# Performance work log

Measured on AMD Instinct MI355X. Metric: run time of the kernel, lower is better.

The kernel has to match this reference:

```python
import jax, jax.numpy as jnp
import numpy as np

N_NODES = 10000
N_EDGES = 80000
F_IN = 128
H1 = 2048
H2 = 2048
H3 = 1024


def _sgconv(x, pos, src, dst, W_in, b_in, W_out, b_out):
    # geo-GCN SpatialGraphConv with hidden_size=1:
    # message(j->i) = relu(Linear(pos_j - pos_i)) * x_j ; aggr='add' ; then Linear out
    rel = pos[src] - pos[dst]                      # [E, 2]  (pos_j - pos_i)
    scale = jax.nn.relu(rel @ W_in + b_in)         # [E, C_in]
    msg = scale * x[src]                           # [E, C_in]
    agg = jax.ops.segment_sum(msg, dst, num_segments=x.shape[0])  # [N, C_in]
    return agg @ W_out + b_out                     # [N, C_out]


def setup_inputs() -> dict:
    key = jax.random.key(0)
    ks = jax.random.split(key, 12)
    x = jax.random.normal(ks[0], (N_NODES, F_IN), dtype=jnp.float32)
    pos = jax.random.normal(ks[1], (N_NODES, 2), dtype=jnp.float32)
    edge_index = jax.random.randint(ks[2], (2, N_EDGES), 0, N_NODES, dtype=jnp.int32)

    def lin(k, fan_in, fan_out):
        lim = 1.0 / np.sqrt(fan_in)
        kw, kb = jax.random.split(k)
        W = jax.random.uniform(kw, (fan_in, fan_out), jnp.float32, -lim, lim)
        b = jax.random.uniform(kb, (fan_out,), jnp.float32, -lim, lim)
        return W, b

    W_in1, b_in1 = lin(ks[3], 2, F_IN)
    W_out1, b_out1 = lin(ks[4], F_IN, H1)
    W_in2, b_in2 = lin(ks[5], 2, H1)
    W_out2, b_out2 = lin(ks[6], H1, H2)
    W_in3, b_in3 = lin(ks[7], 2, H2)
    W_out3, b_out3 = lin(ks[8], H2, H3)

    return {
        "x": x, "pos": pos, "edge_index": edge_index,
        "W_in1": W_in1, "b_in1": b_in1, "W_out1": W_out1, "b_out1": b_out1,
        "W_in2": W_in2, "b_in2": b_in2, "W_out2": W_out2, "b_out2": b_out2,
        "W_in3": W_in3, "b_in3": b_in3, "W_out3": W_out3, "b_out3": b_out3,
    }


def reference(x, pos, edge_index,
              W_in1, b_in1, W_out1, b_out1,
              W_in2, b_in2, W_out2, b_out2,
              W_in3, b_in3, W_out3, b_out3):
    src, dst = edge_index[0], edge_index[1]  # flow source_to_target: j=src, i=dst
    h = jax.nn.relu(_sgconv(x, pos, src, dst, W_in1, b_in1, W_out1, b_out1))
    h = jax.nn.relu(_sgconv(h, pos, src, dst, W_in2, b_in2, W_out2, b_out2))
    h = jax.nn.relu(_sgconv(h, pos, src, dst, W_in3, b_in3, W_out3, b_out3))
    # F.normalize(h, dim=1): L2 normalize rows with eps clamp 1e-12
    norm = jnp.linalg.norm(h, axis=1, keepdims=True)
    return h / jnp.maximum(norm, 1e-12)
```

## Files before the change

### kernel.cpp

```cpp
#include <hip/hip_runtime.h>
#include <hip/hip_bf16.h>

#define DEVI __device__ __forceinline__

constexpr int NN = 10000;
constexpr int NE = 80000;
constexpr int AGG_ROWS = 10240;
constexpr int ES_CAP = 110016;

typedef __attribute__((ext_vector_type(8))) short bf16x8;
typedef __attribute__((ext_vector_type(4))) float f32x4;

DEVI float blo(unsigned int u) {
  union { unsigned int i; float f; } c; c.i = u << 16; return c.f;
}
DEVI float bhi(unsigned int u) {
  union { unsigned int i; float f; } c; c.i = u & 0xffff0000u; return c.f;
}
DEVI unsigned short f2b(float f) {
  union { float f; unsigned int i; } c; c.f = f;
  unsigned int i = c.i;
  return (unsigned short)((i + 0x7fffu + ((i >> 16) & 1u)) >> 16);
}
DEVI void st1(float* p, float v) { *p = v; }
DEVI void st1(unsigned short* p, float v) { *p = f2b(v); }
DEVI void store8b(unsigned short* p, const float v[8]) {
  int4 pk;
  pk.x = (int)((unsigned)f2b(v[0]) | ((unsigned)f2b(v[1]) << 16));
  pk.y = (int)((unsigned)f2b(v[2]) | ((unsigned)f2b(v[3]) << 16));
  pk.z = (int)((unsigned)f2b(v[4]) | ((unsigned)f2b(v[5]) << 16));
  pk.w = (int)((unsigned)f2b(v[6]) | ((unsigned)f2b(v[7]) << 16));
  *reinterpret_cast<int4*>(p) = pk;
}

DEVI void gload16(const void* g, void* l) {
  __builtin_amdgcn_global_load_lds(
      (const __attribute__((address_space(1))) void*)g,
      (__attribute__((address_space(3))) void*)l, 16, 0, 0);
}

__global__ __launch_bounds__(256)
void hist_kernel(const int* __restrict__ dst, int* __restrict__ cnt) {
  int e = blockIdx.x * 256 + threadIdx.x;
  if (e < NE) atomicAdd(&cnt[dst[e]], 1);
}

__global__ __launch_bounds__(1024)
void scan_kernel(const int* __restrict__ cnt, int* __restrict__ off,
                 int* __restrict__ cursor) {
  __shared__ int wpart[16];
  __shared__ int carry;
  int tid = threadIdx.x, lane = tid & 63, w = tid >> 6;
  if (tid == 0) carry = 0;
  __syncthreads();
  for (int base = 0; base < NN; base += 1024) {
    int i = base + tid;
    int v = (i < NN) ? ((cnt[i] + 3) & ~3) : 0;
    int s = v;
#pragma unroll
    for (int o = 1; o < 64; o <<= 1) { int t = __shfl_up(s, o); if (lane >= o) s += t; }
    if (lane == 63) wpart[w] = s;
    __syncthreads();
    if (w == 0) {
      int ws = (lane < 16) ? wpart[lane] : 0;
#pragma unroll
      for (int o = 1; o < 16; o <<= 1) { int t = __shfl_up(ws, o); if (lane >= o) ws += t; }
      if (lane < 16) wpart[lane] = ws;
    }
    __syncthreads();
    int ex = carry + (w ? wpart[w - 1] : 0) + s - v;
    if (i < NN) { off[i] = ex; cursor[i] = ex; }
    __syncthreads();
    if (tid == 0) carry += wpart[15];
    __syncthreads();
  }
}

__global__ __launch_bounds__(256)
void bucket_kernel(const int* __restrict__ src, const int* __restrict__ dst,
                   const float* __restrict__ pos,
                   int* __restrict__ cursor, int* __restrict__ es,
                   float* __restrict__ rel) {
  int e = blockIdx.x * 256 + threadIdx.x;
  if (e < NE) {
    int s = src[e], d = dst[e];
    int p = atomicAdd(&cursor[d], 1);
    float2 ps = *reinterpret_cast<const float2*>(pos + 2 * s);
    float2 pd = *reinterpret_cast<const float2*>(pos + 2 * d);
    es[p] = s;
    *reinterpret_cast<float2*>(rel + 2 * p) = make_float2(ps.x - pd.x, ps.y - pd.y);
  }
}

__global__ __launch_bounds__(256)
void transpose_w(const float* __restrict__ W, unsigned short* __restrict__ WT,
                 int K, int N) {
  __shared__ float tile[32][33];
  int tx = threadIdx.x & 31, ty = threadIdx.x >> 5;
  int n0 = blockIdx.x * 32, k0 = blockIdx.y * 32;
#pragma unroll
  for (int j = 0; j < 32; j += 8)
    tile[ty + j][tx] = W[(size_t)(k0 + ty + j) * N + n0 + tx];
  __syncthreads();
#pragma unroll
  for (int j = 0; j < 32; j += 8)
    WT[(size_t)(n0 + ty + j) * K + k0 + tx] = f2b(tile[tx][ty + j]);
}

__global__ __launch_bounds__(256)
void gather_l1(const float* __restrict__ x,
               const int* __restrict__ off, const int* __restrict__ cnt,
               const int* __restrict__ es, const float* __restrict__ rel,
               const float* __restrict__ Win, const float* __restrict__ bin,
               unsigned short* __restrict__ agg) {
  constexpr int C = 128;
  int lane = threadIdx.x & 63;
  int i = blockIdx.x * 4 + (threadIdx.x >> 6);
  if (i >= NN) return;
  int c = lane * 2;
  float w00 = Win[c], w01 = Win[c + 1];
  float w10 = Win[C + c], w11 = Win[C + c + 1];
  float b0 = bin[c], b1 = bin[c + 1];
  float a0 = 0.f, a1 = 0.f;
  int s0 = off[i], n = cnt[i];

  for (int k = 0; k < n; k += 4) {
    int4 s4 = *reinterpret_cast<const int4*>(es + s0 + k);
    float4 ra = *reinterpret_cast<const float4*>(rel + 2 * (s0 + k));
    float4 rb = *reinterpret_cast<const float4*>(rel + 2 * (s0 + k) + 4);
    float2 q0 = *reinterpret_cast<const float2*>(x + (size_t)s4.x * C + c);
    float2 q1 = *reinterpret_cast<const float2*>(x + (size_t)s4.y * C + c);
    float2 q2 = *reinterpret_cast<const float2*>(x + (size_t)s4.z * C + c);
    float2 q3 = *reinterpret_cast<const float2*>(x + (size_t)s4.w * C + c);
    {
      float sc0 = fmaxf(fmaf(ra.x, w00, fmaf(ra.y, w10, b0)), 0.f);
      float sc1 = fmaxf(fmaf(ra.x, w01, fmaf(ra.y, w11, b1)), 0.f);
      a0 = fmaf(sc0, q0.x, a0); a1 = fmaf(sc1, q0.y, a1);
    }
    if (k + 1 < n) {
      float sc0 = fmaxf(fmaf(ra.z, w00, fmaf(ra.w, w10, b0)), 0.f);
      float sc1 = fmaxf(fmaf(ra.z, w01, fmaf(ra.w, w11, b1)), 0.f);
      a0 = fmaf(sc0, q1.x, a0); a1 = fmaf(sc1, q1.y, a1);
    }
    if (k + 2 < n) {
      float sc0 = fmaxf(fmaf(rb.x, w00, fmaf(rb.y, w10, b0)), 0.f);
      float sc1 = fmaxf(fmaf(rb.x, w01, fmaf(rb.y, w11, b1)), 0.f);
      a0 = fmaf(sc0, q2.x, a0); a1 = fmaf(sc1, q2.y, a1);
    }
    if (k + 3 < n) {
      float sc0 = fmaxf(fmaf(rb.z, w00, fmaf(rb.w, w10, b0)), 0.f);
      float sc1 = fmaxf(fmaf(rb.z, w01, fmaf(rb.w, w11, b1)), 0.f);
      a0 = fmaf(sc0, q3.x, a0); a1 = fmaf(sc1, q3.y, a1);
    }
  }
  unsigned int pk = (unsigned)f2b(a0) | ((unsigned)f2b(a1) << 16);
  *reinterpret_cast<unsigned int*>(agg + (size_t)i * C + c) = pk;
}

__global__ __launch_bounds__(256)
void gather_chunk(const unsigned short* __restrict__ x,
                  const int* __restrict__ off, const int* __restrict__ cnt,
                  const int* __restrict__ es, const float* __restrict__ rel,
                  const float* __restrict__ Win, const float* __restrict__ bin,
                  unsigned short* __restrict__ agg, int ngb8) {
  constexpr int C = 2048;
  constexpr int V = 8;
  int wgid = blockIdx.x;
  int half = wgid >= ngb8;
  int base = half ? wgid - ngb8 : wgid;
  int chunk = (base & 7) + (half << 3);
  int grp = base >> 3;
  int lane = threadIdx.x & 63;
  int wid = threadIdx.x >> 6;
  int slot = lane >> 4;
  int l16 = lane & 15;
  int i = grp * 16 + wid * 4 + slot;
  int c = chunk * 128 + l16 * V;

  float w0[V], w1[V], bb[V], acc[V];
#pragma unroll
  for (int j = 0; j < V; ++j) {
    w0[j] = Win[c + j]; w1[j] = Win[C + c + j]; bb[j] = bin[c + j]; acc[j] = 0.f;
  }
  int s0 = off[i], n = cnt[i];

  auto fma8 = [&](float rx, float ry, const int4& q) {
    float xv[V] = { blo(q.x), bhi(q.x), blo(q.y), bhi(q.y),
                    blo(q.z), bhi(q.z), blo(q.w), bhi(q.w) };
#pragma unroll
    for (int j = 0; j < V; ++j) {
      float sc = fmaxf(fmaf(rx, w0[j], fmaf(ry, w1[j], bb[j])), 0.f);
      acc[j] = fmaf(sc, xv[j], acc[j]);
    }
  };
  for (int k = 0; k < n; k += 4) {
    int4 s4 = *reinterpret_cast<const int4*>(es + s0 + k);
    float4 ra = *reinterpret_cast<const float4*>(rel + 2 * (s0 + k));
    float4 rb = *reinterpret_cast<const float4*>(rel + 2 * (s0 + k) + 4);
    int4 q0 = *reinterpret_cast<const int4*>(x + (size_t)s4.x * C + c);
    int4 q1 = *reinterpret_cast<const int4*>(x + (size_t)s4.y * C + c);
    int4 q2 = *reinterpret_cast<const int4*>(x + (size_t)s4.z * C + c);
    int4 q3 = *reinterpret_cast<const int4*>(x + (size_t)s4.w * C + c);
    fma8(ra.x, ra.y, q0);
    if (k + 1 < n) fma8(ra.z, ra.w, q1);
    if (k + 2 < n) fma8(rb.x, rb.y, q2);
    if (k + 3 < n) fma8(rb.z, rb.w, q3);
  }
  store8b(agg + (size_t)i * C + c, acc);
}

template <typename OT>
__global__ __launch_bounds__(256, 2)
void gemm320(const unsigned short* __restrict__ A,
             const unsigned short* __restrict__ BT,
             const float* __restrict__ bias, OT* __restrict__ out,
             int M, int N, int K) {
  __shared__ unsigned short lds[2 * 14336];
  const int t = threadIdx.x;
  const int lane = t & 63, wid = t >> 6;
  const int wr = wid >> 1, wc = wid & 1;

  const int nwg = gridDim.x * gridDim.y;
  const int orig = blockIdx.y * gridDim.x + blockIdx.x;
  const int swz = (orig & 7) * (nwg >> 3) + (orig >> 3);
  const int bx = swz % gridDim.x, by = swz / gridDim.x;
  const int m0 = by * 320, n0 = bx * 128;
  const int nk = K >> 5;

  const int lrow = lane >> 2;
  const int schunk = (lane & 3) ^ ((lrow >> 1) & 3);
  const unsigned short* gA = A + (size_t)(m0 + wid * 80 + lrow) * K + schunk * 8;
  const unsigned short* gB = BT + (size_t)(n0 + wid * 32 + lrow) * K + schunk * 8;
  const int lA0 = wid * 5 * 512 + lane * 8;
  const int lB0 = 10240 + wid * 2 * 512 + lane * 8;

  auto STAGE = [&](int buf, int kt) {
    const unsigned short* ga = gA + kt * 32;
    const unsigned short* gb = gB + kt * 32;
    unsigned short* la = lds + buf * 14336 + lA0;
    unsigned short* lb = lds + buf * 14336 + lB0;
#pragma unroll
    for (int jj = 0; jj < 5; ++jj)
      gload16(ga + (size_t)(jj * 16) * K, la + jj * 512);
#pragma unroll
    for (int jj = 0; jj < 2; ++jj)
      gload16(gb + (size_t)(jj * 16) * K, lb + jj * 512);
  };

  const int frow = lane & 15;
  const int fslot = ((lane >> 4) ^ ((frow >> 1) & 3)) * 8;
  const int paOff = (wr * 160 + frow) * 32 + fslot;
  const int pbOff = 10240 + (wc * 64 + frow) * 32 + fslot;

  f32x4 acc[10][4];
#pragma unroll
  for (int m = 0; m < 10; ++m)
#pragma unroll
    for (int n = 0; n < 4; ++n) acc[m][n] = 0.f;

  STAGE(0, 0);

  int cur = 0;
  for (int kt = 0; kt < nk; ++kt) {
    if (kt + 1 < nk) {
      STAGE(cur ^ 1, kt + 1);
      asm volatile("s_waitcnt vmcnt(7)" ::: "memory");
    } else {
      asm volatile("s_waitcnt vmcnt(0)" ::: "memory");
    }
    asm volatile("s_barrier" ::: "memory");
    const unsigned short* pa = lds + cur * 14336 + paOff;
    const unsigned short* pb = lds + cur * 14336 + pbOff;
    bf16x8 bf[4];
#pragma unroll
    for (int n = 0; n < 4; ++n)
      bf[n] = *reinterpret_cast<const bf16x8*>(pb + n * 512);
    __builtin_amdgcn_s_setprio(1);
#pragma unroll
    for (int m = 0; m < 10; ++m) {
      bf16x8 af = *reinterpret_cast<const bf16x8*>(pa + m * 512);
#pragma unroll
      for (int n = 0; n < 4; ++n)
        acc[m][n] = __builtin_amdgcn_mfma_f32_16x16x32_bf16(
            af, bf[n], acc[m][n], 0, 0, 0);
    }
    __builtin_amdgcn_s_setprio(0);
    asm volatile("s_barrier" ::: "memory");
    cur ^= 1;
  }

  const int ccol = lane & 15;
  const int crow = (lane >> 4) * 4;
  float bv[4];
#pragma unroll
  for (int n = 0; n < 4; ++n)
    bv[n] = bias[n0 + wc * 64 + n * 16 + ccol];
#pragma unroll
  for (int m = 0; m < 10; ++m) {
    int gm0 = m0 + wr * 160 + m * 16 + crow;
#pragma unroll
    for (int r = 0; r < 4; ++r) {
      int gm = gm0 + r;
      if (gm < M) {
        size_t base = (size_t)gm * N + n0 + wc * 64 + ccol;
#pragma unroll
        for (int n = 0; n < 4; ++n)
          st1(out + base + n * 16, fmaxf(acc[m][n][r] + bv[n], 0.f));
      }
    }
  }
}

__global__ __launch_bounds__(256)
void l2norm_kernel(float* __restrict__ out) {
  constexpr int C = 1024;
  float* p = out + (size_t)blockIdx.x * C;
  float4 v = *reinterpret_cast<const float4*>(p + threadIdx.x * 4);
  float s = v.x * v.x + v.y * v.y + v.z * v.z + v.w * v.w;
#pragma unroll
  for (int o = 32; o > 0; o >>= 1) s += __shfl_down(s, o);
  __shared__ float wsum[4];
  if ((threadIdx.x & 63) == 0) wsum[threadIdx.x >> 6] = s;
  __syncthreads();
  float tot = wsum[0] + wsum[1] + wsum[2] + wsum[3];
  float inv = 1.0f / fmaxf(sqrtf(tot), 1e-12f);
  float4 r = make_float4(v.x * inv, v.y * inv, v.z * inv, v.w * inv);
  *reinterpret_cast<float4*>(p + threadIdx.x * 4) = r;
}

extern "C" void kernel_launch(void* const* d_in, const int* in_sizes, int n_in,
                              void* d_out, int out_size, void* d_ws, size_t ws_size,
                              hipStream_t stream) {
  (void)in_sizes; (void)n_in; (void)out_size; (void)ws_size;
  const float* x     = (const float*)d_in[0];
  const float* pos   = (const float*)d_in[1];
  const int*   ei    = (const int*)d_in[2];
  const int*   srcv  = ei;
  const int*   dstv  = ei + NE;
  const float* Win1  = (const float*)d_in[3];
  const float* bin1  = (const float*)d_in[4];
  const float* Wout1 = (const float*)d_in[5];
  const float* bout1 = (const float*)d_in[6];
  const float* Win2  = (const float*)d_in[7];
  const float* bin2  = (const float*)d_in[8];
  const float* Wout2 = (const float*)d_in[9];
  const float* bout2 = (const float*)d_in[10];
  const float* Win3  = (const float*)d_in[11];
  const float* bin3  = (const float*)d_in[12];
  const float* Wout3 = (const float*)d_in[13];
  const float* bout3 = (const float*)d_in[14];
  float* outp = (float*)d_out;

  char* ws = (char*)d_ws;
  unsigned short* aggb = (unsigned short*)ws;
  unsigned short* h1   = (unsigned short*)(ws + 41943040);
  unsigned short* W2T  = (unsigned short*)(ws + 82903040);
  unsigned short* W3T  = (unsigned short*)(ws + 91291648);
  unsigned short* W1T  = (unsigned short*)(ws + 95485952);
  int* cnt    = (int*)(ws + 96010240);
  int* off    = (int*)(ws + 96050240);
  int* cursor = (int*)(ws + 96090240);
  int* es     = (int*)(ws + 96130240);
  float* rel  = (float*)(ws + 96570304);
  unsigned short* h2 = (unsigned short*)d_out;

  const dim3 blk(256);
  const int eb = (NE + 255) / 256;
  const int ngb8 = ((NN + 15) / 16) * 8;

  hipMemsetAsync(cnt, 0, NN * sizeof(int), stream);
  hipMemsetAsync(es, 0, ES_CAP * sizeof(int), stream);
  hist_kernel<<<eb, blk, 0, stream>>>(dstv, cnt);
  scan_kernel<<<1, 1024, 0, stream>>>(cnt, off, cursor);
  bucket_kernel<<<eb, blk, 0, stream>>>(srcv, dstv, pos, cursor, es, rel);

  transpose_w<<<dim3(2048 / 32, 128 / 32),  blk, 0, stream>>>(Wout1, W1T, 128, 2048);
  transpose_w<<<dim3(2048 / 32, 2048 / 32), blk, 0, stream>>>(Wout2, W2T, 2048, 2048);
  transpose_w<<<dim3(1024 / 32, 2048 / 32), blk, 0, stream>>>(Wout3, W3T, 2048, 1024);

  hipMemsetAsync(aggb + (size_t)NN * 2048, 0, (size_t)(AGG_ROWS - NN) * 2048 * 2, stream);

  gather_l1<<<(NN + 3) / 4, blk, 0, stream>>>(x, off, cnt, es, rel, Win1, bin1, aggb);
  gemm320<unsigned short><<<dim3(2048 / 128, AGG_ROWS / 320), blk, 0, stream>>>(
      aggb, W1T, bout1, h1, NN, 2048, 128);

  gather_chunk<<<2 * ngb8, blk, 0, stream>>>(h1, off, cnt, es, rel, Win2, bin2, aggb, ngb8);
  gemm320<unsigned short><<<dim3(2048 / 128, AGG_ROWS / 320), blk, 0, stream>>>(
      aggb, W2T, bout2, h2, NN, 2048, 2048);

  gather_chunk<<<2 * ngb8, blk, 0, stream>>>(h2, off, cnt, es, rel, Win3, bin3, aggb, ngb8);
  gemm320<float><<<dim3(1024 / 128, AGG_ROWS / 320), blk, 0, stream>>>(
      aggb, W3T, bout3, outp, NN, 1024, 2048);

  l2norm_kernel<<<NN, blk, 0, stream>>>(outp);
}
```

Baseline: 324.9 us.

## Split GEMM tile across eight waves with dedicated A and B loader waves

The 320x128 GEMM block now runs 512 threads instead of 256. Each wave computes an 80x64 sub-tile instead of 160x64, which halves its accumulator registers and is meant to allow more resident waves to hide latency. Staging is reassigned so waves 0-3 load A rows and waves 4-7 load B rows, and each wave waits on its own matching vmcnt. The trade-off is that B fragments are read from LDS by twice as many waves, and each wave does less MFMA work per barrier.

```diff
diff --git a/kernel.cpp b/kernel.cpp
--- a/kernel.cpp
+++ b/kernel.cpp
@@ -210,7 +210,7 @@
 }
 
 template <typename OT>
-__global__ __launch_bounds__(256, 2)
+__global__ __launch_bounds__(512, 4)
 void gemm320(const unsigned short* __restrict__ A,
              const unsigned short* __restrict__ BT,
              const float* __restrict__ bias, OT* __restrict__ out,
@@ -229,32 +229,36 @@
 
   const int lrow = lane >> 2;
   const int schunk = (lane & 3) ^ ((lrow >> 1) & 3);
-  const unsigned short* gA = A + (size_t)(m0 + wid * 80 + lrow) * K + schunk * 8;
-  const unsigned short* gB = BT + (size_t)(n0 + wid * 32 + lrow) * K + schunk * 8;
-  const int lA0 = wid * 5 * 512 + lane * 8;
-  const int lB0 = 10240 + wid * 2 * 512 + lane * 8;
+  const bool isA = wid < 4;
+  const int aw = wid & 3;
+  const unsigned short* gSrc = isA
+      ? A + (size_t)(m0 + aw * 80 + lrow) * K + schunk * 8
+      : BT + (size_t)(n0 + aw * 32 + lrow) * K + schunk * 8;
+  const int lBase = isA ? (aw * 5 * 512 + lane * 8)
+                        : (10240 + aw * 2 * 512 + lane * 8);
 
   auto STAGE = [&](int buf, int kt) {
-    const unsigned short* ga = gA + kt * 32;
-    const unsigned short* gb = gB + kt * 32;
-    unsigned short* la = lds + buf * 14336 + lA0;
-    unsigned short* lb = lds + buf * 14336 + lB0;
-#pragma unroll
-    for (int jj = 0; jj < 5; ++jj)
-      gload16(ga + (size_t)(jj * 16) * K, la + jj * 512);
-#pragma unroll
-    for (int jj = 0; jj < 2; ++jj)
-      gload16(gb + (size_t)(jj * 16) * K, lb + jj * 512);
+    const unsigned short* g = gSrc + kt * 32;
+    unsigned short* l = lds + buf * 14336 + lBase;
+    if (isA) {
+#pragma unroll
+      for (int jj = 0; jj < 5; ++jj)
+        gload16(g + (size_t)(jj * 16) * K, l + jj * 512);
+    } else {
+#pragma unroll
+      for (int jj = 0; jj < 2; ++jj)
+        gload16(g + (size_t)(jj * 16) * K, l + jj * 512);
+    }
   };
 
   const int frow = lane & 15;
   const int fslot = ((lane >> 4) ^ ((frow >> 1) & 3)) * 8;
-  const int paOff = (wr * 160 + frow) * 32 + fslot;
+  const int paOff = (wr * 80 + frow) * 32 + fslot;
   const int pbOff = 10240 + (wc * 64 + frow) * 32 + fslot;
 
-  f32x4 acc[10][4];
-#pragma unroll
-  for (int m = 0; m < 10; ++m)
+  f32x4 acc[5][4];
+#pragma unroll
+  for (int m = 0; m < 5; ++m)
 #pragma unroll
     for (int n = 0; n < 4; ++n) acc[m][n] = 0.f;
 
@@ -264,7 +268,8 @@
   for (int kt = 0; kt < nk; ++kt) {
     if (kt + 1 < nk) {
       STAGE(cur ^ 1, kt + 1);
-      asm volatile("s_waitcnt vmcnt(7)" ::: "memory");
+      if (isA) asm volatile("s_waitcnt vmcnt(5)" ::: "memory");
+      else     asm volatile("s_waitcnt vmcnt(2)" ::: "memory");
     } else {
       asm volatile("s_waitcnt vmcnt(0)" ::: "memory");
     }
@@ -277,7 +282,7 @@
       bf[n] = *reinterpret_cast<const bf16x8*>(pb + n * 512);
     __builtin_amdgcn_s_setprio(1);
 #pragma unroll
-    for (int m = 0; m < 10; ++m) {
+    for (int m = 0; m < 5; ++m) {
       bf16x8 af = *reinterpret_cast<const bf16x8*>(pa + m * 512);
 #pragma unroll
       for (int n = 0; n < 4; ++n)
@@ -296,8 +301,8 @@
   for (int n = 0; n < 4; ++n)
     bv[n] = bias[n0 + wc * 64 + n * 16 + ccol];
 #pragma unroll
-  for (int m = 0; m < 10; ++m) {
-    int gm0 = m0 + wr * 160 + m * 16 + crow;
+  for (int m = 0; m < 5; ++m) {
+    int gm0 = m0 + wr * 80 + m * 16 + crow;
 #pragma unroll
     for (int r = 0; r < 4; ++r) {
       int gm = gm0 + r;
@@ -381,15 +386,15 @@
   hipMemsetAsync(aggb + (size_t)NN * 2048, 0, (size_t)(AGG_ROWS - NN) * 2048 * 2, stream);
 
   gather_l1<<<(NN + 3) / 4, blk, 0, stream>>>(x, off, cnt, es, rel, Win1, bin1, aggb);
-  gemm320<unsigned short><<<dim3(2048 / 128, AGG_ROWS / 320), blk, 0, stream>>>(
+  gemm320<unsigned short><<<dim3(2048 / 128, AGG_ROWS / 320), 512, 0, stream>>>(
       aggb, W1T, bout1, h1, NN, 2048, 128);
 
   gather_chunk<<<2 * ngb8, blk, 0, stream>>>(h1, off, cnt, es, rel, Win2, bin2, aggb, ngb8);
-  gemm320<unsigned short><<<dim3(2048 / 128, AGG_ROWS / 320), blk, 0, stream>>>(
+  gemm320<unsigned short><<<dim3(2048 / 128, AGG_ROWS / 320), 512, 0, stream>>>(
       aggb, W2T, bout2, h2, NN, 2048, 2048);
 
   gather_chunk<<<2 * ngb8, blk, 0, stream>>>(h2, off, cnt, es, rel, Win3, bin3, aggb, ngb8);
-  gemm320<float><<<dim3(1024 / 128, AGG_ROWS / 320), blk, 0, stream>>>(
+  gemm320<float><<<dim3(1024 / 128, AGG_ROWS / 320), 512, 0, stream>>>(
       aggb, W3T, bout3, outp, NN, 1024, 2048);
 
   l2norm_kernel<<<NN, blk, 0, stream>>>(outp);
```

Measured after the change: 317.5 us. -2.3%, faster.
